# Optimization experiments

Measured on AMD Instinct MI355X. Metric: run time of the kernel, lower is better.

## Reference

```python
import jax, jax.numpy as jnp
import numpy as np

N_HEADS = 16

def setup_inputs() -> dict:
    key = jax.random.key(0)
    qkv = jax.random.normal(key, (4, 3072, 1024), dtype=jnp.float32)
    return {"qkv": qkv}

def reference(qkv):
    bs, width, length = qkv.shape
    ch = width // (3 * N_HEADS)
    qkv_h = qkv.reshape(bs * N_HEADS, 3 * ch, length)
    q, k, v = jnp.split(qkv_h, 3, axis=1)  # each [bs*H, ch, T]
    scale = 1.0 / jnp.sqrt(jnp.sqrt(jnp.asarray(ch, qkv.dtype)))
    # [bs*H, T, T] scores
    weight = jnp.einsum('bct,bcs->bts', q * scale, k * scale)
    weight = jax.nn.softmax(weight.astype(jnp.float32), axis=-1).astype(weight.dtype)
    a = jnp.einsum('bts,bcs->bct', weight, v)  # [bs*H, ch, T]
    return a.reshape(bs, -1, length)
```

## Files before the change

### kernel.cpp

```cpp
#include <hip/hip_runtime.h>
#include <hip/hip_bf16.h>


typedef __bf16 bf16_8 __attribute__((ext_vector_type(8)));
typedef __bf16 bf16_4 __attribute__((ext_vector_type(4)));
typedef float floatx4 __attribute__((ext_vector_type(4)));

#define NTHREADS 256
#define STR 64
#define NSTEPS 16

#if __has_builtin(__builtin_amdgcn_exp2f)
#define EXP2(x) __builtin_amdgcn_exp2f(x)
#else
#define EXP2(x) exp2f(x)
#endif
#define QSCALE 0.18033688011112042f

#define LDS_BYTES 49152

__device__ __forceinline__ int kap(int row) { return ((row >> 1) + (row >> 4)) & 7; }

__global__ __launch_bounds__(NTHREADS, 2)
void attn_kernel(const float* __restrict__ qkv, float* __restrict__ out) {
    __shared__ char smem[LDS_BYTES];
    __bf16* q_s = (__bf16*)smem;
    __bf16* k0  = (__bf16*)(smem + 16384);
    __bf16* k1  = (__bf16*)(smem + 24576);
    __bf16* v0  = (__bf16*)(smem + 32768);
    __bf16* v1  = (__bf16*)(smem + 40960);

    const int tid  = threadIdx.x;
    const int wave = tid >> 6;
    const int lane = tid & 63;
    const int quad = lane >> 4;
    const int i16  = lane & 15;

    const int bx = blockIdx.x;
    const int bh = bx & 63;
    const int t0 = (bx >> 6) << 7;

    const float* qg = qkv + (size_t)bh * 196608;
    const float* kg = qg + 65536;
    const float* vg = qg + 131072;

    const int si = tid & 15;
    const int sG = tid >> 4;
    const int c0 = sG << 2;

    #pragma unroll
    for (int j = 0; j < 2; ++j) {
        int f  = j * NTHREADS + tid;
        int cG = f >> 5;
        int ti = f & 31;
        float4 q4[4];
        #pragma unroll
        for (int jj = 0; jj < 4; ++jj)
            q4[jj] = *(const float4*)(qg + (cG * 4 + jj) * 1024 + t0 + ti * 4);
        #pragma unroll
        for (int rr = 0; rr < 4; ++rr) {
            int trow = ti * 4 + rr;
            bf16_4 w;
            w[0] = (__bf16)(((const float*)&q4[0])[rr] * QSCALE);
            w[1] = (__bf16)(((const float*)&q4[1])[rr] * QSCALE);
            w[2] = (__bf16)(((const float*)&q4[2])[rr] * QSCALE);
            w[3] = (__bf16)(((const float*)&q4[3])[rr] * QSCALE);
            *(bf16_4*)&q_s[trow * STR + ((cG ^ (kap(trow) << 1)) << 2)] = w;
        }
    }
    {
        float4 k4[4], v4[4];
        #pragma unroll
        for (int jj = 0; jj < 4; ++jj) {
            k4[jj] = *(const float4*)(kg + (c0 + jj) * 1024 + si * 4);
            v4[jj] = *(const float4*)(vg + (c0 + jj) * 1024 + si * 4);
        }
        #pragma unroll
        for (int rr = 0; rr < 4; ++rr) {
            int srow = si * 4 + rr;
            bf16_4 w;
            w[0] = (__bf16)((const float*)&k4[0])[rr];
            w[1] = (__bf16)((const float*)&k4[1])[rr];
            w[2] = (__bf16)((const float*)&k4[2])[rr];
            w[3] = (__bf16)((const float*)&k4[3])[rr];
            *(bf16_4*)&k0[srow * STR + ((sG ^ (kap(srow) << 1)) << 2)] = w;
        }
        #pragma unroll
        for (int jj = 0; jj < 4; ++jj) {
            int c = c0 + jj;
            bf16_4 w;
            w[0] = (__bf16)v4[jj].x; w[1] = (__bf16)v4[jj].y;
            w[2] = (__bf16)v4[jj].z; w[3] = (__bf16)v4[jj].w;
            *(bf16_4*)&v0[c * STR + ((si ^ (kap(c) << 1)) << 2)] = w;
        }
    }
    __syncthreads();

    bf16_8 qf[2][2];
    #pragma unroll
    for (int tt = 0; tt < 2; ++tt) {
        int row = wave * 32 + tt * 16 + i16;
        int x = kap(row);
        #pragma unroll
        for (int kk = 0; kk < 2; ++kk)
            qf[tt][kk] = *(const bf16_8*)&q_s[row * STR + ((((kk << 2) | quad) ^ x) << 3)];
    }

    floatx4 O[2][4];
    #pragma unroll
    for (int tt = 0; tt < 2; ++tt)
        #pragma unroll
        for (int cn = 0; cn < 4; ++cn) O[tt][cn] = (floatx4){0.f, 0.f, 0.f, 0.f};
    float l[2] = {0.f, 0.f};

    __bf16* pw = q_s + (size_t)(wave * 32) * STR;
    const int xp0 = (i16 >> 1) & 7;
    const int xv  = 0;

    for (int is = 0; is < NSTEPS; ++is) {
        const __bf16* kc = (is & 1) ? k1 : k0;
        const __bf16* vc = (is & 1) ? v1 : v0;

        float4 kr[4], vr[4];
        if (is < NSTEPS - 1) {
            const int s0n = (is + 1) * 64;
            #pragma unroll
            for (int jj = 0; jj < 4; ++jj) {
                kr[jj] = *(const float4*)(kg + (c0 + jj) * 1024 + s0n + si * 4);
                vr[jj] = *(const float4*)(vg + (c0 + jj) * 1024 + s0n + si * 4);
            }
        }

        floatx4 St[2][4];
        #pragma unroll
        for (int sb = 0; sb < 4; ++sb) {
            int srow = sb * 16 + i16;
            int x = (sb + (i16 >> 1)) & 7;
            bf16_8 kf0 = *(const bf16_8*)&kc[srow * STR + ((quad ^ x) << 3)];
            bf16_8 kf1 = *(const bf16_8*)&kc[srow * STR + (((4 | quad) ^ x) << 3)];
            floatx4 a0 = (floatx4){0.f, 0.f, 0.f, 0.f};
            floatx4 a1 = (floatx4){0.f, 0.f, 0.f, 0.f};
            a0 = __builtin_amdgcn_mfma_f32_16x16x32_bf16(kf0, qf[0][0], a0, 0, 0, 0);
            a0 = __builtin_amdgcn_mfma_f32_16x16x32_bf16(kf1, qf[0][1], a0, 0, 0, 0);
            a1 = __builtin_amdgcn_mfma_f32_16x16x32_bf16(kf0, qf[1][0], a1, 0, 0, 0);
            a1 = __builtin_amdgcn_mfma_f32_16x16x32_bf16(kf1, qf[1][1], a1, 0, 0, 0);
            St[0][sb] = a0;
            St[1][sb] = a1;
        }
        #pragma unroll
        for (int tt = 0; tt < 2; ++tt) {
            int trow = tt * 16 + i16;
            int xp = (tt + xp0) & 7;
            #pragma unroll
            for (int sb = 0; sb < 4; ++sb) {
                float p0 = EXP2(St[tt][sb][0]);
                float p1 = EXP2(St[tt][sb][1]);
                float p2 = EXP2(St[tt][sb][2]);
                float p3 = EXP2(St[tt][sb][3]);
                l[tt] += (p0 + p1) + (p2 + p3);
                bf16_4 pk;
                pk[0] = (__bf16)p0; pk[1] = (__bf16)p1;
                pk[2] = (__bf16)p2; pk[3] = (__bf16)p3;
                int ch = ((sb << 2) | quad) ^ (xp << 1);
                *(bf16_4*)&pw[trow * STR + (ch << 2)] = pk;
            }
        }
        bf16_8 af[2][2];
        #pragma unroll
        for (int tt = 0; tt < 2; ++tt) {
            int trow = tt * 16 + i16;
            int xp = (tt + xp0) & 7;
            #pragma unroll
            for (int kk = 0; kk < 2; ++kk)
                af[tt][kk] = *(const bf16_8*)&pw[trow * STR + ((((kk << 2) | quad) ^ xp) << 3)];
        }
        #pragma unroll
        for (int cn = 0; cn < 4; ++cn) {
            int crow = cn * 16 + i16;
            int xc = (cn + (i16 >> 1)) & 7;
            #pragma unroll
            for (int kk = 0; kk < 2; ++kk) {
                bf16_8 vf = *(const bf16_8*)&vc[crow * STR + ((((kk << 2) | quad) ^ xc) << 3)];
                O[0][cn] = __builtin_amdgcn_mfma_f32_16x16x32_bf16(vf, af[0][kk], O[0][cn], 0, 0, 0);
                O[1][cn] = __builtin_amdgcn_mfma_f32_16x16x32_bf16(vf, af[1][kk], O[1][cn], 0, 0, 0);
            }
        }

        if (is < NSTEPS - 1) {
            __bf16* kn = (is & 1) ? k0 : k1;
            __bf16* vn = (is & 1) ? v0 : v1;
            #pragma unroll
            for (int rr = 0; rr < 4; ++rr) {
                int srow = si * 4 + rr;
                bf16_4 w;
                w[0] = (__bf16)((const float*)&kr[0])[rr];
                w[1] = (__bf16)((const float*)&kr[1])[rr];
                w[2] = (__bf16)((const float*)&kr[2])[rr];
                w[3] = (__bf16)((const float*)&kr[3])[rr];
                *(bf16_4*)&kn[srow * STR + ((sG ^ (kap(srow) << 1)) << 2)] = w;
            }
            #pragma unroll
            for (int jj = 0; jj < 4; ++jj) {
                int c = c0 + jj;
                bf16_4 w;
                w[0] = (__bf16)vr[jj].x; w[1] = (__bf16)vr[jj].y;
                w[2] = (__bf16)vr[jj].z; w[3] = (__bf16)vr[jj].w;
                *(bf16_4*)&vn[c * STR + ((si ^ (kap(c) << 1)) << 2)] = w;
            }
        }
        __syncthreads();
    }

    float* og = out + (size_t)bh * 65536 + t0 + wave * 32;
    #pragma unroll
    for (int tt = 0; tt < 2; ++tt) {
        float s = l[tt];
        s += __shfl_xor(s, 16);
        s += __shfl_xor(s, 32);
        const float linv = 1.0f / s;
        #pragma unroll
        for (int cn = 0; cn < 4; ++cn)
            #pragma unroll
            for (int r = 0; r < 4; ++r)
                og[(cn * 16 + 4 * quad + r) * 1024 + tt * 16 + i16] = O[tt][cn][r] * linv;
    }
}

extern "C" void kernel_launch(void* const* d_in, const int* in_sizes, int n_in,
                              void* d_out, int out_size, void* d_ws, size_t ws_size,
                              hipStream_t stream) {
    const float* qkv = (const float*)d_in[0];
    float* out = (float*)d_out;
    attn_kernel<<<dim3(512), dim3(NTHREADS), 0, stream>>>(qkv, out);
}
```

Baseline: 106.3 us.

## Defer PV MFMA by one step with triple-buffered V tiles

Each step's P·V MFMA is moved into the next loop iteration, using P fragments carried in registers. This lets the PV matrix products overlap the QK^T and exp work of the following tile. V tiles now rotate through three LDS buffers so the deferred step can still read the previous V while the next one is written, and a tail block handles the last tile. LDS use grows by 8 KB per block, which could affect occupancy, and register pressure rises from carrying the fragments.

Result: no change. 105.8 us (-0.5%).

```diff
diff --git a/kernel.cpp b/kernel.cpp
--- a/kernel.cpp
+++ b/kernel.cpp
@@ -17,7 +17,7 @@
 #endif
 #define QSCALE 0.18033688011112042f
 
-#define LDS_BYTES 49152
+#define LDS_BYTES 57344
 
 __device__ __forceinline__ int kap(int row) { return ((row >> 1) + (row >> 4)) & 7; }
 
@@ -29,6 +29,7 @@
     __bf16* k1  = (__bf16*)(smem + 24576);
     __bf16* v0  = (__bf16*)(smem + 32768);
     __bf16* v1  = (__bf16*)(smem + 40960);
+    __bf16* v2  = (__bf16*)(smem + 49152);
 
     const int tid  = threadIdx.x;
     const int wave = tid >> 6;
@@ -115,11 +116,12 @@
 
     __bf16* pw = q_s + (size_t)(wave * 32) * STR;
     const int xp0 = (i16 >> 1) & 7;
-    const int xv  = 0;
+
+    bf16_8 afp[2][2];
+    int vprev = 2, vcur = 0, vnext = 1;
 
     for (int is = 0; is < NSTEPS; ++is) {
         const __bf16* kc = (is & 1) ? k1 : k0;
-        const __bf16* vc = (is & 1) ? v1 : v0;
 
         float4 kr[4], vr[4];
         if (is < NSTEPS - 1) {
@@ -174,21 +176,30 @@
             for (int kk = 0; kk < 2; ++kk)
                 af[tt][kk] = *(const bf16_8*)&pw[trow * STR + ((((kk << 2) | quad) ^ xp) << 3)];
         }
-        #pragma unroll
-        for (int cn = 0; cn < 4; ++cn) {
-            int crow = cn * 16 + i16;
-            int xc = (cn + (i16 >> 1)) & 7;
-            #pragma unroll
-            for (int kk = 0; kk < 2; ++kk) {
-                bf16_8 vf = *(const bf16_8*)&vc[crow * STR + ((((kk << 2) | quad) ^ xc) << 3)];
-                O[0][cn] = __builtin_amdgcn_mfma_f32_16x16x32_bf16(vf, af[0][kk], O[0][cn], 0, 0, 0);
-                O[1][cn] = __builtin_amdgcn_mfma_f32_16x16x32_bf16(vf, af[1][kk], O[1][cn], 0, 0, 0);
-            }
-        }
+
+        if (is > 0) {
+            const __bf16* vp = (vprev == 0) ? v0 : ((vprev == 1) ? v1 : v2);
+            #pragma unroll
+            for (int cn = 0; cn < 4; ++cn) {
+                int crow = cn * 16 + i16;
+                int xc = (cn + (i16 >> 1)) & 7;
+                #pragma unroll
+                for (int kk = 0; kk < 2; ++kk) {
+                    bf16_8 vf = *(const bf16_8*)&vp[crow * STR + ((((kk << 2) | quad) ^ xc) << 3)];
+                    O[0][cn] = __builtin_amdgcn_mfma_f32_16x16x32_bf16(vf, afp[0][kk], O[0][cn], 0, 0, 0);
+                    O[1][cn] = __builtin_amdgcn_mfma_f32_16x16x32_bf16(vf, afp[1][kk], O[1][cn], 0, 0, 0);
+                }
+            }
+        }
+        #pragma unroll
+        for (int tt = 0; tt < 2; ++tt)
+            #pragma unroll
+            for (int kk = 0; kk < 2; ++kk)
+                afp[tt][kk] = af[tt][kk];
 
         if (is < NSTEPS - 1) {
             __bf16* kn = (is & 1) ? k0 : k1;
-            __bf16* vn = (is & 1) ? v0 : v1;
+            __bf16* vn = (vnext == 0) ? v0 : ((vnext == 1) ? v1 : v2);
             #pragma unroll
             for (int rr = 0; rr < 4; ++rr) {
                 int srow = si * 4 + rr;
@@ -207,8 +218,24 @@
                 w[2] = (__bf16)vr[jj].z; w[3] = (__bf16)vr[jj].w;
                 *(bf16_4*)&vn[c * STR + ((si ^ (kap(c) << 1)) << 2)] = w;
             }
-        }
-        __syncthreads();
+            __syncthreads();
+        }
+        vprev = vcur; vcur = vnext; vnext = (vnext == 2) ? 0 : vnext + 1;
+    }
+
+    {
+        const __bf16* vp = (vprev == 0) ? v0 : ((vprev == 1) ? v1 : v2);
+        #pragma unroll
+        for (int cn = 0; cn < 4; ++cn) {
+            int crow = cn * 16 + i16;
+            int xc = (cn + (i16 >> 1)) & 7;
+            #pragma unroll
+            for (int kk = 0; kk < 2; ++kk) {
+                bf16_8 vf = *(const bf16_8*)&vp[crow * STR + ((((kk << 2) | quad) ^ xc) << 3)];
+                O[0][cn] = __builtin_amdgcn_mfma_f32_16x16x32_bf16(vf, afp[0][kk], O[0][cn], 0, 0, 0);
+                O[1][cn] = __builtin_amdgcn_mfma_f32_16x16x32_bf16(vf, afp[1][kk], O[1][cn], 0, 0, 0);
+            }
+        }
     }
 
     float* og = out + (size_t)bh * 65536 + t0 + wave * 32;
```
